# Performance work log

Hardware: AMD Instinct MI355X
Metric: run time of the kernel (lower is better)

The kernel has to match this reference:

```python
import jax, jax.numpy as jnp
import numpy as np

N, D, E = 200000, 256, 6400000
RATIO = 0.5
NEG_SLOPE = 0.2


def _xavier(key, shape, gain=1.414):
    fan_in, fan_out = shape[0], shape[1]
    limit = gain * (6.0 / (fan_in + fan_out)) ** 0.5
    return jax.random.uniform(key, shape, jnp.float32, -limit, limit)


def setup_inputs() -> dict:
    key = jax.random.key(0)
    ks = jax.random.split(key, 8)
    x = jax.random.normal(ks[0], (N, D), jnp.float32)
    edge_index = jax.random.randint(ks[1], (2, E), 0, N, dtype=jnp.int64)
    return {
        "x": x,
        "edge_index": edge_index,
        "w_s1": _xavier(ks[2], (2 * D, D)), "b_s1": jnp.zeros((D,), jnp.float32),
        "w_s2": _xavier(ks[3], (D, 1)),     "b_s2": jnp.zeros((1,), jnp.float32),
        "w_f1": _xavier(ks[4], (D, D // 2)), "b_f1": jnp.zeros((D // 2,), jnp.float32),
        "w_f2": _xavier(ks[5], (D // 2, 1)), "b_f2": jnp.zeros((1,), jnp.float32),
        "w_p": _xavier(ks[6], (D, D)),      "b_p": jnp.zeros((D,), jnp.float32),
        "alpha": jnp.float32(0.5), "beta": jnp.float32(0.5),
    }


def reference(x, edge_index, w_s1, b_s1, w_s2, b_s2, w_f1, b_f1, w_f2, b_f2, w_p, b_p, alpha, beta):
    num_nodes = x.shape[0]
    k = max(1, int(RATIO * num_nodes))
    lrelu = lambda v: jax.nn.leaky_relu(v, NEG_SLOPE)

    row, col = edge_index[0], edge_index[1]
    # degree(row, N): scatter-add of ones over source nodes
    deg = jax.ops.segment_sum(jnp.ones_like(row, dtype=x.dtype), row, num_segments=num_nodes)
    # F.normalize(p=2, dim=0) on the [N,1] degree column
    deg_norm = deg / jnp.maximum(jnp.sqrt(jnp.sum(deg * deg)), 1e-12)

    struct_in = jnp.concatenate([x, jnp.broadcast_to(deg_norm[:, None], x.shape)], axis=1)  # [N, 2D]
    struct_scores = (lrelu(struct_in @ w_s1 + b_s1) @ w_s2 + b_s2)[:, 0]  # dropout is eval no-op
    feat_scores = (lrelu(x @ w_f1 + b_f1) @ w_f2 + b_f2)[:, 0]

    a = jax.nn.sigmoid(alpha)
    b = jax.nn.sigmoid(beta)
    s = a + b
    scores = (a / s) * struct_scores + (b / s) * feat_scores  # [N]

    # single-graph top-k (batch=None default path)
    topk_scores, topk_idx = jax.lax.top_k(scores, k)
    x_pooled = lrelu(x[topk_idx] @ w_p + b_p)  # post_pool, dropout no-op

    # edge remap + compaction (valid edges first, -1 padding to keep static shape)
    node_map = jnp.full((num_nodes,), -1, dtype=jnp.int32).at[topk_idx].set(
        jnp.arange(k, dtype=jnp.int32))
    mr, mc = node_map[row], node_map[col]
    mask = (mr >= 0) & (mc >= 0)
    order = jnp.argsort(~mask, stable=True)  # stable: keeps original edge order among valid
    edge_index_pooled = jnp.stack([
        jnp.where(mask, mr, -1)[order],
        jnp.where(mask, mc, -1)[order],
    ])
    return x_pooled, edge_index_pooled, topk_scores
```

## Files before the change

### kernel.cpp

```cpp
#include <hip/hip_runtime.h>
#include <math.h>

typedef unsigned long long u64;
typedef unsigned int u32;
typedef unsigned short u16;
typedef __attribute__((ext_vector_type(8))) short bf16x8;
typedef __attribute__((ext_vector_type(4))) float f32x4;

#define D   256
#define ECH 16
#define EBLK (256*ECH)
#define BAND_W 4096
#define BAND_DELTA 1e-3f
#define HR  12544
#define HCH 32

__device__ __forceinline__ double lrelu(double v){ return v > 0.0 ? v : 0.2*v; }
__device__ __forceinline__ float  lreluf(float v){ return v > 0.0f ? v : 0.2f*v; }

__device__ __forceinline__ u16 f2bf(float f){
  union{float f; u32 u;} v; v.f = f;
  u32 r = v.u + 0x7FFFu + ((v.u >> 16) & 1u);
  return (u16)(r >> 16);
}
__device__ __forceinline__ float bf2f(u16 b){
  union{u32 u; float f;} v; v.u = ((u32)b) << 16; return v.f;
}

__global__ __launch_bounds__(256) void k_deghist(const int* __restrict__ row, int E,
                                                 u32* __restrict__ partial, int NR){
  __shared__ u32 h[HR];
  const int tid = threadIdx.x;
  const int r = blockIdx.x % NR;
  const int c = blockIdx.x / NR;
  for (int i = tid; i < HR; i += 256) h[i] = 0;
  __syncthreads();
  const int lo = r * HR;
  int CE = ((E + HCH - 1) / HCH + 3) & ~3;
  const int e0 = c * CE;
  const int e1 = min(e0 + CE, E);
  for (int e = e0 + tid*4; e < e1; e += 256*4){
    if (e + 3 < e1){
      int4 v = *(const int4*)(row + e);
      u32 d0 = (u32)(v.x - lo), d1 = (u32)(v.y - lo);
      u32 d2 = (u32)(v.z - lo), d3 = (u32)(v.w - lo);
      if (d0 < (u32)HR) atomicAdd(&h[d0], 1u);
      if (d1 < (u32)HR) atomicAdd(&h[d1], 1u);
      if (d2 < (u32)HR) atomicAdd(&h[d2], 1u);
      if (d3 < (u32)HR) atomicAdd(&h[d3], 1u);
    } else {
      for (int j = 0; j < 4 && e + j < e1; ++j){
        u32 d = (u32)(row[e+j] - lo);
        if (d < (u32)HR) atomicAdd(&h[d], 1u);
      }
    }
  }
  __syncthreads();
  u32* plane = partial + (size_t)blockIdx.x * HR;
  for (int i = tid; i < HR; i += 256) plane[i] = h[i];
}

__global__ void k_degred2(const u32* __restrict__ partial, int N, int NR,
                          int* __restrict__ deg, u64* __restrict__ out){
  __shared__ u64 sh[256];
  u64 local = 0;
  int stride = gridDim.x*blockDim.x;
  for (int i = blockIdx.x*blockDim.x + threadIdx.x; i < N; i += stride){
    int r = i / HR, off = i % HR;
    u32 s = 0;
    #pragma unroll 8
    for (int c = 0; c < HCH; ++c) s += partial[(size_t)(c*NR + r)*HR + off];
    deg[i] = (int)s;
    local += (u64)s * (u64)s;
  }
  sh[threadIdx.x] = local; __syncthreads();
  for (int s = 128; s > 0; s >>= 1){
    if (threadIdx.x < s) sh[threadIdx.x] += sh[threadIdx.x+s];
    __syncthreads();
  }
  if (threadIdx.x == 0) atomicAdd(out, sh[0]);
}

__global__ void k_prep(const float* __restrict__ wS1, const float* __restrict__ alpha,
                       const float* __restrict__ beta, const u64* __restrict__ sumsq,
                       double* __restrict__ s1b, double* __restrict__ scal,
                       float* __restrict__ s1bf, float* __restrict__ scalf){
  int j = threadIdx.x;
  double s = 0.0;
  for (int r = 0; r < D; ++r) s += (double)wS1[(D + r)*D + j];
  s1b[j] = s;
  s1bf[j] = (float)s;
  if (j == 0){
    double a = 1.0/(1.0 + exp(-(double)alpha[0]));
    double b = 1.0/(1.0 + exp(-(double)beta[0]));
    scal[0] = a/(a+b);
    scal[1] = b/(a+b);
    double dn = sqrt((double)(*sumsq));
    scal[2] = dn > 1e-12 ? dn : 1e-12;
    scalf[0] = (float)scal[0];
    scalf[1] = (float)scal[1];
    scalf[2] = (float)(1.0/scal[2]);
  }
}

__global__ void k_wsw(const float* __restrict__ wS1, const float* __restrict__ wF1,
                      u16* __restrict__ wswH, u16* __restrict__ wswL){
  int idx = blockIdx.x*blockDim.x + threadIdx.x;
  int i    = idx & 7;
  int lane = (idx >> 3) & 63;
  int sg   = (idx >> 9) & 7;
  int t    = idx >> 12;
  int k = sg*32 + ((lane >> 4) & 3)*8 + i;
  int c16 = lane & 15;
  float wv;
  if (t < 16) wv = wS1[k*256 + t*16 + c16];
  else        wv = wF1[k*128 + (t-16)*16 + c16];
  u16 h = f2bf(wv);
  float lo = wv - bf2f(h);
  wswH[idx] = h;
  wswL[idx] = f2bf(lo);
}

__global__ void k_wswP(const float* __restrict__ wP,
                       u16* __restrict__ wH, u16* __restrict__ wL){
  int idx = blockIdx.x*blockDim.x + threadIdx.x;
  int i    = idx & 7;
  int lane = (idx >> 3) & 63;
  int sg   = (idx >> 9) & 7;
  int t    = idx >> 12;
  int k = sg*32 + ((lane >> 4) & 3)*8 + i;
  float wv = wP[k*256 + t*16 + (lane & 15)];
  u16 h = f2bf(wv);
  float lo = wv - bf2f(h);
  wH[idx] = h;
  wL[idx] = f2bf(lo);
}

__global__ __launch_bounds__(512, 4) void k_scores_mfma(
    const float* __restrict__ x, const int* __restrict__ deg,
    const u16* __restrict__ wswH, const u16* __restrict__ wswL,
    const float* __restrict__ bS1, const float* __restrict__ wS2, const float* __restrict__ bS2,
    const float* __restrict__ bF1, const float* __restrict__ wF2, const float* __restrict__ bF2,
    const float* __restrict__ s1bf, const float* __restrict__ scalf,
    float* __restrict__ s32, u64* __restrict__ keys, int N)
{
  __shared__ u16 xsh[2][4096];
  __shared__ u16 xsl[2][4096];
  __shared__ float dnsh[64];
  __shared__ float part_s[64][9];
  __shared__ float part_f[64][9];

  const int tid  = threadIdx.x;
  const int lane = tid & 63;
  const int w    = tid >> 6;
  const int node0 = blockIdx.x * 64;

  if (tid < 64){
    int node = node0 + tid;
    dnsh[tid] = (node < N) ? ((float)deg[node] * scalf[2]) : 0.0f;
  }

  const int row_st = tid >> 3;
  const int seg_st = tid & 7;
  const int unit_w = row_st*8 + (seg_st ^ (row_st & 7));
  const float* srcbase = x + (size_t)(node0 + row_st)*D + seg_st*8;
  const bool rv = (node0 + row_st) < N;

  f32x4 acc[4][3];
  #pragma unroll
  for (int m = 0; m < 4; ++m)
    #pragma unroll
    for (int n = 0; n < 3; ++n) acc[m][n] = (f32x4){0.f,0.f,0.f,0.f};

  float xr[8];
  {
    if (rv){
      float4 a = *(const float4*)(srcbase);
      float4 b = *(const float4*)(srcbase + 4);
      xr[0]=a.x; xr[1]=a.y; xr[2]=a.z; xr[3]=a.w;
      xr[4]=b.x; xr[5]=b.y; xr[6]=b.z; xr[7]=b.w;
    } else {
      #pragma unroll
      for (int i = 0; i < 8; ++i) xr[i] = 0.f;
    }
  }

  #pragma unroll
  for (int c = 0; c < 4; ++c){
    const int pb = c & 1;
    {
      u16 h[8];
      #pragma unroll
      for (int i = 0; i < 8; ++i) h[i] = f2bf(xr[i]);
      uint4 H; H.x = (u32)h[0] | ((u32)h[1]<<16); H.y = (u32)h[2] | ((u32)h[3]<<16);
               H.z = (u32)h[4] | ((u32)h[5]<<16); H.w = (u32)h[6] | ((u32)h[7]<<16);
      u16 l[8];
      #pragma unroll
      for (int i = 0; i < 8; ++i) l[i] = f2bf(xr[i] - bf2f(h[i]));
      uint4 L; L.x = (u32)l[0] | ((u32)l[1]<<16); L.y = (u32)l[2] | ((u32)l[3]<<16);
               L.z = (u32)l[4] | ((u32)l[5]<<16); L.w = (u32)l[6] | ((u32)l[7]<<16);
      *(uint4*)&xsh[pb][unit_w*8] = H;
      *(uint4*)&xsl[pb][unit_w*8] = L;
    }
    if (c < 3){
      const float* sn = srcbase + (c+1)*64;
      if (rv){
        float4 a = *(const float4*)(sn);
        float4 b = *(const float4*)(sn + 4);
        xr[0]=a.x; xr[1]=a.y; xr[2]=a.z; xr[3]=a.w;
        xr[4]=b.x; xr[5]=b.y; xr[6]=b.z; xr[7]=b.w;
      }
    }
    __syncthreads();
    #pragma unroll
    for (int s = 0; s < 2; ++s){
      const int sg = c*2 + s;
      bf16x8 ah[4], al[4];
      #pragma unroll
      for (int mt = 0; mt < 4; ++mt){
        int row = mt*16 + (lane & 15);
        int seg = s*4 + (lane >> 4);
        int un  = row*8 + (seg ^ (row & 7));
        ah[mt] = *(const bf16x8*)&xsh[pb][un*8];
        al[mt] = *(const bf16x8*)&xsl[pb][un*8];
      }
      const int t0 = w*3;
      size_t o0 = ((size_t)(t0*8 + sg)*64 + lane)*8;
      bf16x8 bh = *(const bf16x8*)&wswH[o0];
      bf16x8 bl = *(const bf16x8*)&wswL[o0];
      #pragma unroll
      for (int nt = 0; nt < 3; ++nt){
        bf16x8 nbh = bh, nbl = bl;
        if (nt < 2){
          size_t on = ((size_t)((t0+nt+1)*8 + sg)*64 + lane)*8;
          nbh = *(const bf16x8*)&wswH[on];
          nbl = *(const bf16x8*)&wswL[on];
        }
        #pragma unroll
        for (int mt = 0; mt < 4; ++mt){
          acc[mt][nt] = __builtin_amdgcn_mfma_f32_16x16x32_bf16(ah[mt], bh, acc[mt][nt], 0,0,0);
          acc[mt][nt] = __builtin_amdgcn_mfma_f32_16x16x32_bf16(al[mt], bh, acc[mt][nt], 0,0,0);
          acc[mt][nt] = __builtin_amdgcn_mfma_f32_16x16x32_bf16(ah[mt], bl, acc[mt][nt], 0,0,0);
        }
        bh = nbh; bl = nbl;
      }
    }
    __syncthreads();
  }

  float dnl[4][4];
  #pragma unroll
  for (int mt = 0; mt < 4; ++mt)
    #pragma unroll
    for (int j = 0; j < 4; ++j)
      dnl[mt][j] = dnsh[mt*16 + (lane>>4)*4 + j];

  float ps[4][4], pf[4][4];
  #pragma unroll
  for (int mt = 0; mt < 4; ++mt)
    #pragma unroll
    for (int j = 0; j < 4; ++j){ ps[mt][j] = 0.f; pf[mt][j] = 0.f; }

  #pragma unroll
  for (int nt = 0; nt < 3; ++nt){
    const int t = w*3 + nt;
    const int c16 = lane & 15;
    const bool isS = (t < 16);
    const int col = isS ? t*16 + c16 : (t-16)*16 + c16;
    const float bias = isS ? bS1[col] : bF1[col];
    const float sbv  = isS ? s1bf[col] : 0.f;
    const float vv   = isS ? wS2[col] : wF2[col];
    #pragma unroll
    for (int mt = 0; mt < 4; ++mt){
      #pragma unroll
      for (int j = 0; j < 4; ++j){
        float v = acc[mt][nt][j] + bias + dnl[mt][j]*sbv;
        v = lreluf(v) * vv;
        v += __shfl_xor(v, 1);
        v += __shfl_xor(v, 2);
        v += __shfl_xor(v, 4);
        v += __shfl_xor(v, 8);
        if (isS) ps[mt][j] += v; else pf[mt][j] += v;
      }
    }
  }
  if ((lane & 15) == 0){
    #pragma unroll
    for (int mt = 0; mt < 4; ++mt)
      #pragma unroll
      for (int j = 0; j < 4; ++j){
        int row = mt*16 + (lane>>4)*4 + j;
        part_s[row][w] = ps[mt][j];
        part_f[row][w] = pf[mt][j];
      }
  }
  __syncthreads();
  if (tid < 64){
    int node = node0 + tid;
    if (node < N){
      float sv = 0.f, fv = 0.f;
      #pragma unroll
      for (int ww = 0; ww < 8; ++ww){ sv += part_s[tid][ww]; fv += part_f[tid][ww]; }
      float sc = scalf[0]*(sv + bS2[0]) + scalf[1]*(fv + bF2[0]);
      s32[node] = sc;
      u32 bits = __float_as_uint(sc);
      u32 ord = (bits >> 31) ? ~bits : (bits | 0x80000000u);
      keys[node] = ((u64)(~ord) << 32) | (u32)node;
    }
  }
}

__global__ void k_padkeys(u64* __restrict__ keys, int N, int SORTN){
  int i = N + blockIdx.x*blockDim.x + threadIdx.x;
  if (i < SORTN) keys[i] = ~0ULL;
}

__global__ __launch_bounds__(1024) void k_bsort_local8k(u64* __restrict__ keys){
  __shared__ u64 sk[8192];
  const int tid = threadIdx.x;
  const int base = blockIdx.x * 8192;
  #pragma unroll
  for (int e = 0; e < 8; ++e) sk[tid + e*1024] = keys[base + tid + e*1024];
  __syncthreads();
  for (int size = 2; size <= 8192; size <<= 1){
    for (int stride = size >> 1; stride > 0; stride >>= 1){
      #pragma unroll
      for (int pp = 0; pp < 4; ++pp){
        int p  = tid + pp*1024;
        int i  = 2*p - (p & (stride-1));
        int jj = i + stride;
        bool up = (((base + i) & size) == 0);
        u64 ki = sk[i], kj = sk[jj];
        if ((ki > kj) == up){ sk[i] = kj; sk[jj] = ki; }
      }
      __syncthreads();
    }
  }
  #pragma unroll
  for (int e = 0; e < 8; ++e) keys[base + tid + e*1024] = sk[tid + e*1024];
}

__global__ __launch_bounds__(1024) void k_bmerge_local8k(u64* __restrict__ keys, int size){
  __shared__ u64 sk[8192];
  const int tid = threadIdx.x;
  const int base = blockIdx.x * 8192;
  #pragma unroll
  for (int e = 0; e < 8; ++e) sk[tid + e*1024] = keys[base + tid + e*1024];
  __syncthreads();
  for (int stride = 4096; stride > 0; stride >>= 1){
    #pragma unroll
    for (int pp = 0; pp < 4; ++pp){
      int p  = tid + pp*1024;
      int i  = 2*p - (p & (stride-1));
      int jj = i + stride;
      bool up = (((base + i) & size) == 0);
      u64 ki = sk[i], kj = sk[jj];
      if ((ki > kj) == up){ sk[i] = kj; sk[jj] = ki; }
    }
    __syncthreads();
  }
  #pragma unroll
  for (int e = 0; e < 8; ++e) keys[base + tid + e*1024] = sk[tid + e*1024];
}

template<int NS>
__global__ void k_bpassM(u64* __restrict__ keys, int size, int stride){
  const int G = 1 << NS;
  u32 t = blockIdx.x*blockDim.x + threadIdx.x;
  u32 smin = (u32)stride >> (NS-1);
  u32 i0 = (t/smin)*(smin << NS) + (t % smin);
  u64 v[G];
  #pragma unroll
  for (int j = 0; j < G; ++j) v[j] = keys[i0 + (u32)j*smin];
  bool up = ((i0 & (u32)size) == 0);
  #pragma unroll
  for (int b = (G>>1); b >= 1; b >>= 1){
    #pragma unroll
    for (int j = 0; j < G; ++j){
      if ((j & b) == 0){
        u64 a = v[j], cc = v[j|b];
        if ((a > cc) == up){ v[j] = cc; v[j|b] = a; }
      }
    }
  }
  #pragma unroll
  for (int j = 0; j < G; ++j) keys[i0 + (u32)j*smin] = v[j];
}

__global__ void kr_cut(const u64* __restrict__ keys, int k, float* __restrict__ cutbuf,
                       int* __restrict__ r01){
  if (threadIdx.x == 0 && blockIdx.x == 0){
    u32 key32 = (u32)(keys[k-1] >> 32);
    u32 ord = ~key32;
    u32 u = (ord & 0x80000000u) ? (ord ^ 0x80000000u) : ~ord;
    float c = __uint_as_float(u);
    cutbuf[0] = c - BAND_DELTA;
    cutbuf[1] = c + BAND_DELTA;
    r01[0] = 0x7FFFFFFF;
    r01[1] = -1;
  }
}

__global__ __launch_bounds__(256) void kr_rescore(
    const u64* __restrict__ keys, const float* __restrict__ s32,
    const float* __restrict__ x, const int* __restrict__ deg,
    const float* __restrict__ wS1, const float* __restrict__ bS1,
    const float* __restrict__ wS2, const float* __restrict__ bS2,
    const float* __restrict__ wF1, const float* __restrict__ bF1,
    const float* __restrict__ wF2, const float* __restrict__ bF2,
    const double* __restrict__ s1b, const double* __restrict__ scal,
    const float* __restrict__ cutbuf, int* __restrict__ r01,
    double* __restrict__ bandS, int k, int N)
{
  const int r = k - BAND_W + blockIdx.x;
  if (r < 0 || r >= N) return;
  const int node = (int)(u32)(keys[r] & 0xFFFFFFFFULL);
  const float s = s32[node];
  if (s < cutbuf[0] || s > cutbuf[1]) return;

  const int tid = threadIdx.x;
  if (tid == 0){ atomicMin(&r01[0], r); atomicMax(&r01[1], r); }

  __shared__ float xr[256];
  __shared__ double rsp[4], rfp[4];
  xr[tid] = x[(size_t)node*D + tid];
  __syncthreads();

  const int j = tid;
  double accA = (double)bS1[j] + ((double)deg[node]/scal[2]) * s1b[j];
  double accB = (j < 128) ? (double)bF1[j] : 0.0;
  for (int rr = 0; rr < D; ++rr){
    double xv = (double)xr[rr];
    accA = fma(xv, (double)wS1[rr*D + j], accA);
    if (j < 128) accB = fma(xv, (double)wF1[rr*128 + j], accB);
  }
  double sp = lrelu(accA) * (double)wS2[j];
  double fp = (j < 128) ? lrelu(accB) * (double)wF2[j] : 0.0;

  const int lane = tid & 63, wave = tid >> 6;
  #pragma unroll
  for (int off = 32; off > 0; off >>= 1){
    sp += __shfl_down(sp, off);
    fp += __shfl_down(fp, off);
  }
  if (lane == 0){ rsp[wave] = sp; rfp[wave] = fp; }
  __syncthreads();
  if (tid == 0){
    double SP = rsp[0]+rsp[1]+rsp[2]+rsp[3];
    double FP = rfp[0]+rfp[1]+rfp[2]+rfp[3];
    bandS[blockIdx.x] = scal[0]*(SP + (double)bS2[0]) + scal[1]*(FP + (double)bF2[0]);
  }
}

__global__ __launch_bounds__(1024) void kr_bandsort(u64* __restrict__ keys,
    const double* __restrict__ bandS, const int* __restrict__ r01, int k){
  __shared__ double bs[8192];
  __shared__ int bi[8192];
  const int r0 = r01[0], r1 = r01[1];
  int nb = r1 - r0 + 1;
  if (nb <= 1) return;
  if (nb > 8192) nb = 8192;
  int M = 1; while (M < nb) M <<= 1;
  const int tid = threadIdx.x;
  const int sbase = r0 - (k - BAND_W);
  for (int m = tid; m < M; m += 1024){
    if (m < nb){ bs[m] = bandS[sbase + m]; bi[m] = (int)(u32)(keys[r0+m] & 0xFFFFFFFFULL); }
    else       { bs[m] = -1.0/0.0;         bi[m] = 0x7FFFFFFF; }
  }
  __syncthreads();
  for (int size = 2; size <= M; size <<= 1){
    for (int stride = size >> 1; stride > 0; stride >>= 1){
      for (int p = tid; p < (M >> 1); p += 1024){
        int i = 2*p - (p & (stride-1));
        int jj = i + stride;
        bool up = ((i & size) == 0);
        double si_ = bs[i], sj = bs[jj];
        int ii = bi[i], ij = bi[jj];
        bool gt = (si_ < sj) || (si_ == sj && ii > ij);
        if (gt == up){ bs[i]=sj; bs[jj]=si_; bi[i]=ij; bi[jj]=ii; }
      }
      __syncthreads();
    }
  }
  for (int m = tid; m < nb; m += 1024)
    keys[r0+m] = (u64)(u32)bi[m];
}

__global__ void k_finalize(const u64* __restrict__ keys, const float* __restrict__ s32,
                           int k, int* __restrict__ nmap, float* __restrict__ outS){
  int p = blockIdx.x*blockDim.x + threadIdx.x;
  if (p < k){
    int node = (int)(u32)(keys[p] & 0xFFFFFFFFULL);
    nmap[node] = p;
    outS[p] = s32[node];
  }
}

__global__ __launch_bounds__(512, 4) void k_xpool_mfma(
    const float* __restrict__ x, const u64* __restrict__ keys,
    const u16* __restrict__ wH, const u16* __restrict__ wL,
    const float* __restrict__ bP, float* __restrict__ out, int kk)
{
  __shared__ u16 xsh[2][4096];
  __shared__ u16 xsl[2][4096];

  const int tid  = threadIdx.x;
  const int lane = tid & 63;
  const int w    = tid >> 6;
  const int p0 = blockIdx.x * 64;
  if (p0 >= kk) return;

  const int row_st = tid >> 3;
  const int seg_st = tid & 7;
  const int unit_w = row_st*8 + (seg_st ^ (row_st & 7));
  int prow = p0 + row_st; if (prow >= kk) prow = kk - 1;
  const int node = (int)(u32)(keys[prow] & 0xFFFFFFFFULL);
  const float* srcbase = x + (size_t)node*D + seg_st*8;

  f32x4 acc[4][2];
  #pragma unroll
  for (int m = 0; m < 4; ++m){ acc[m][0] = (f32x4){0.f,0.f,0.f,0.f}; acc[m][1] = (f32x4){0.f,0.f,0.f,0.f}; }

  float xr[8];
  {
    float4 a = *(const float4*)(srcbase);
    float4 b = *(const float4*)(srcbase + 4);
    xr[0]=a.x; xr[1]=a.y; xr[2]=a.z; xr[3]=a.w;
    xr[4]=b.x; xr[5]=b.y; xr[6]=b.z; xr[7]=b.w;
  }

  #pragma unroll
  for (int c = 0; c < 4; ++c){
    const int pb = c & 1;
    {
      u16 h[8];
      #pragma unroll
      for (int i = 0; i < 8; ++i) h[i] = f2bf(xr[i]);
      uint4 H; H.x = (u32)h[0] | ((u32)h[1]<<16); H.y = (u32)h[2] | ((u32)h[3]<<16);
               H.z = (u32)h[4] | ((u32)h[5]<<16); H.w = (u32)h[6] | ((u32)h[7]<<16);
      u16 l[8];
      #pragma unroll
      for (int i = 0; i < 8; ++i) l[i] = f2bf(xr[i] - bf2f(h[i]));
      uint4 L; L.x = (u32)l[0] | ((u32)l[1]<<16); L.y = (u32)l[2] | ((u32)l[3]<<16);
               L.z = (u32)l[4] | ((u32)l[5]<<16); L.w = (u32)l[6] | ((u32)l[7]<<16);
      *(uint4*)&xsh[pb][unit_w*8] = H;
      *(uint4*)&xsl[pb][unit_w*8] = L;
    }
    if (c < 3){
      const float* sn = srcbase + (c+1)*64;
      float4 a = *(const float4*)(sn);
      float4 b = *(const float4*)(sn + 4);
      xr[0]=a.x; xr[1]=a.y; xr[2]=a.z; xr[3]=a.w;
      xr[4]=b.x; xr[5]=b.y; xr[6]=b.z; xr[7]=b.w;
    }
    __syncthreads();
    #pragma unroll
    for (int s = 0; s < 2; ++s){
      const int sg = c*2 + s;
      bf16x8 ah[4], al[4];
      #pragma unroll
      for (int mt = 0; mt < 4; ++mt){
        int row = mt*16 + (lane & 15);
        int seg = s*4 + (lane >> 4);
        int un  = row*8 + (seg ^ (row & 7));
        ah[mt] = *(const bf16x8*)&xsh[pb][un*8];
        al[mt] = *(const bf16x8*)&xsl[pb][un*8];
      }
      const int t0 = w*2;
      size_t o0 = ((size_t)(t0*8 + sg)*64 + lane)*8;
      bf16x8 bh = *(const bf16x8*)&wH[o0];
      bf16x8 bl = *(const bf16x8*)&wL[o0];
      #pragma unroll
      for (int nt = 0; nt < 2; ++nt){
        bf16x8 nbh = bh, nbl = bl;
        if (nt < 1){
          size_t on = ((size_t)((t0+1)*8 + sg)*64 + lane)*8;
          nbh = *(const bf16x8*)&wH[on];
          nbl = *(const bf16x8*)&wL[on];
        }
        #pragma unroll
        for (int mt = 0; mt < 4; ++mt){
          acc[mt][nt] = __builtin_amdgcn_mfma_f32_16x16x32_bf16(ah[mt], bh, acc[mt][nt], 0,0,0);
          acc[mt][nt] = __builtin_amdgcn_mfma_f32_16x16x32_bf16(al[mt], bh, acc[mt][nt], 0,0,0);
          acc[mt][nt] = __builtin_amdgcn_mfma_f32_16x16x32_bf16(ah[mt], bl, acc[mt][nt], 0,0,0);
        }
        bh = nbh; bl = nbl;
      }
    }
    __syncthreads();
  }

  const int c16 = lane & 15, r4 = (lane >> 4)*4;
  #pragma unroll
  for (int nt = 0; nt < 2; ++nt){
    const int col = (w*2 + nt)*16 + c16;
    const float bias = bP[col];
    #pragma unroll
    for (int mt = 0; mt < 4; ++mt){
      #pragma unroll
      for (int j = 0; j < 4; ++j){
        int p = p0 + mt*16 + r4 + j;
        if (p < kk) out[(size_t)p*D + col] = lreluf(acc[mt][nt][j] + bias);
      }
    }
  }
}

__global__ __launch_bounds__(256) void k_ecount(const int* __restrict__ erow, const int* __restrict__ ecol,
    const int* __restrict__ nmap, int E, int* __restrict__ bcount){
  __shared__ int sc[256];
  const int tid = threadIdx.x;
  const int base = blockIdx.x*EBLK + tid*ECH;
  int cnt = 0;
  #pragma unroll
  for (int q = 0; q < ECH; ++q){
    int e = base + q;
    if (e < E){
      if (nmap[erow[e]] >= 0 && nmap[ecol[e]] >= 0) cnt++;
    }
  }
  sc[tid] = cnt; __syncthreads();
  for (int s = 128; s > 0; s >>= 1){
    if (tid < s) sc[tid] += sc[tid+s];
    __syncthreads();
  }
  if (tid == 0) bcount[blockIdx.x] = sc[0];
}

__global__ __launch_bounds__(1024) void k_escan(const int* __restrict__ bcount, int nblk,
                                                int* __restrict__ boff, int* __restrict__ tot){
  __shared__ int sh[1024];
  const int tid = threadIdx.x;
  int carry = 0;
  for (int s = 0; s < nblk; s += 1024){
    int v = (s + tid < nblk) ? bcount[s+tid] : 0;
    sh[tid] = v; __syncthreads();
    for (int d = 1; d < 1024; d <<= 1){
      int t = (tid >= d) ? sh[tid-d] : 0;
      __syncthreads();
      sh[tid] += t;
      __syncthreads();
    }
    if (s + tid < nblk) boff[s+tid] = carry + sh[tid] - v;
    carry += sh[1023];
    __syncthreads();
  }
  if (tid == 0) *tot = carry;
}

__global__ void k_efill_tail(float* __restrict__ outR, float* __restrict__ outC,
                             const int* __restrict__ tot, int E){
  const int t0 = *tot;
  int stride = gridDim.x*blockDim.x;
  for (int i = t0 + blockIdx.x*blockDim.x + threadIdx.x; i < E; i += stride){
    outR[i] = -1.0f;
    outC[i] = -1.0f;
  }
}

__global__ __launch_bounds__(256) void k_escatter(const int* __restrict__ erow, const int* __restrict__ ecol,
    const int* __restrict__ nmap, int E, const int* __restrict__ boff,
    float* __restrict__ outR, float* __restrict__ outC){
  __shared__ int sc[256];
  const int tid = threadIdx.x;
  const int base = blockIdx.x*EBLK + tid*ECH;
  int mr[ECH], mc[ECH];
  int cnt = 0;
  #pragma unroll
  for (int q = 0; q < ECH; ++q){
    int e = base + q;
    int a = -1, b = -1;
    if (e < E){ a = nmap[erow[e]]; b = nmap[ecol[e]]; }
    mr[q] = a; mc[q] = b;
    if (a >= 0 && b >= 0) cnt++;
  }
  sc[tid] = cnt; __syncthreads();
  int v = cnt;
  for (int d = 1; d < 256; d <<= 1){
    int t = (tid >= d) ? sc[tid-d] : 0;
    __syncthreads();
    sc[tid] += t;
    __syncthreads();
  }
  int pos = boff[blockIdx.x] + sc[tid] - v;
  #pragma unroll
  for (int q = 0; q < ECH; ++q){
    if (mr[q] >= 0 && mc[q] >= 0){
      outR[pos] = (float)mr[q];
      outC[pos] = (float)mc[q];
      pos++;
    }
  }
}

extern "C" void kernel_launch(void* const* d_in, const int* in_sizes, int n_in,
                              void* d_out, int out_size, void* d_ws, size_t ws_size,
                              hipStream_t stream)
{
  const float* x   = (const float*)d_in[0];
  const int*   ei  = (const int*)d_in[1];
  const float* wS1 = (const float*)d_in[2];
  const float* bS1 = (const float*)d_in[3];
  const float* wS2 = (const float*)d_in[4];
  const float* bS2 = (const float*)d_in[5];
  const float* wF1 = (const float*)d_in[6];
  const float* bF1 = (const float*)d_in[7];
  const float* wF2 = (const float*)d_in[8];
  const float* bF2 = (const float*)d_in[9];
  const float* wP  = (const float*)d_in[10];
  const float* bP  = (const float*)d_in[11];
  const float* alpha = (const float*)d_in[12];
  const float* beta  = (const float*)d_in[13];
  (void)n_in; (void)out_size; (void)ws_size;

  const int N = in_sizes[0] / D;
  const int E = in_sizes[1] / 2;
  int k = (int)(0.5 * (double)N); if (k < 1) k = 1;
  int SORTN = 8192; while (SORTN < N) SORTN <<= 1;
  const int nblk_e = (E + EBLK - 1) / EBLK;
  const int NR = (N + HR - 1) / HR;

  char* w = (char*)d_ws;
  size_t off = 0;
  auto alloc = [&](size_t bytes)->char*{
    char* p = w + off;
    off = (off + bytes + 255) & ~(size_t)255;
    return p;
  };
  float*  s32    = (float*) alloc((size_t)N*4);
  u64*    keys   = (u64*)   alloc((size_t)SORTN*8);
  int*    deg    = (int*)   alloc((size_t)N*4);
  int*    nmap   = (int*)   alloc((size_t)N*4);
  double* s1b    = (double*)alloc((size_t)D*8);
  float*  s1bf   = (float*) alloc((size_t)D*4);
  double* scal   = (double*)alloc(4*8);
  float*  scalf  = (float*) alloc(4*4);
  u64*    sumsq  = (u64*)   alloc(8);
  float*  cutbuf = (float*) alloc(2*4);
  int*    r01    = (int*)   alloc(2*4);
  int*    tot    = (int*)   alloc(4);
  double* bandS  = (double*)alloc((size_t)2*BAND_W*8);
  u16*    wswH   = (u16*)   alloc((size_t)98304*2);
  u16*    wswL   = (u16*)   alloc((size_t)98304*2);
  u16*    wswPH  = (u16*)   alloc((size_t)65536*2);
  u16*    wswPL  = (u16*)   alloc((size_t)65536*2);
  int*    bcount = (int*)   alloc((size_t)nblk_e*4);
  int*    boff   = (int*)   alloc((size_t)nblk_e*4);

  float* outX  = (float*)d_out;
  float* outER = outX  + (size_t)k*D;
  float* outEC = outER + (size_t)E;
  float* outS  = outEC + (size_t)E;

  u32* partial = (u32*)outER;

  hipMemsetAsync(sumsq, 0,    8,           stream);
  hipMemsetAsync(nmap,  0xFF, (size_t)N*4, stream);

  k_deghist<<<NR*HCH, 256, 0, stream>>>(ei, E, partial, NR);
  k_degred2<<<1024, 256, 0, stream>>>(partial, N, NR, deg, sumsq);
  k_prep   <<<1,    D,   0, stream>>>(wS1, alpha, beta, sumsq, s1b, scal, s1bf, scalf);
  k_wsw    <<<384,  256, 0, stream>>>(wS1, wF1, wswH, wswL);
  k_wswP   <<<256,  256, 0, stream>>>(wP, wswPH, wswPL);
  k_scores_mfma<<<(N + 63)/64, 512, 0, stream>>>(x, deg, wswH, wswL,
                                                 bS1, wS2, bS2, bF1, wF2, bF2,
                                                 s1bf, scalf, s32, keys, N);
  k_padkeys<<<(SORTN - N + 255)/256, 256, 0, stream>>>(keys, N, SORTN);

  k_bsort_local8k<<<SORTN/8192, 1024, 0, stream>>>(keys);
  for (int size = 16384; size <= SORTN; size <<= 1){
    int stride = size >> 1;
    while (stride >= 8192){
      int ns = 1;
      while (ns < 4 && (stride >> ns) >= 8192) ns++;
      switch (ns){
        case 1: k_bpassM<1><<<SORTN/2/256,  256, 0, stream>>>(keys, size, stride); break;
        case 2: k_bpassM<2><<<SORTN/4/256,  256, 0, stream>>>(keys, size, stride); break;
        case 3: k_bpassM<3><<<SORTN/8/256,  256, 0, stream>>>(keys, size, stride); break;
        default:k_bpassM<4><<<SORTN/16/256, 256, 0, stream>>>(keys, size, stride); break;
      }
      stride >>= ns;
    }
    k_bmerge_local8k<<<SORTN/8192, 1024, 0, stream>>>(keys, size);
  }

  kr_cut     <<<1, 64, 0, stream>>>(keys, k, cutbuf, r01);
  kr_rescore <<<2*BAND_W, 256, 0, stream>>>(keys, s32, x, deg, wS1,bS1,wS2,bS2,
                                            wF1,bF1,wF2,bF2, s1b, scal,
                                            cutbuf, r01, bandS, k, N);
  kr_bandsort<<<1, 1024, 0, stream>>>(keys, bandS, r01, k);

  k_finalize<<<(k+255)/256, 256, 0, stream>>>(keys, s32, k, nmap, outS);
  k_xpool_mfma<<<(k+63)/64, 512, 0, stream>>>(x, keys, wswPH, wswPL, bP, outX, k);
  k_ecount  <<<nblk_e, 256, 0, stream>>>(ei, ei+E, nmap, E, bcount);
  k_escan   <<<1, 1024, 0, stream>>>(bcount, nblk_e, boff, tot);
  k_efill_tail<<<1024, 256, 0, stream>>>(outER, outEC, tot, E);
  k_escatter<<<nblk_e, 256, 0, stream>>>(ei, ei+E, nmap, E, boff, outER, outEC);
}
```

Measured before the change: 828.8 us.

## Stage full x tile in LDS once and use 2x4 warp grid for MFMA GEMMs

Both the score kernel and the post-pool projection kernel now load and split the whole 64x256 input tile into LDS in one pass with a single barrier, replacing the double-buffered four-chunk pipeline. Warps are rearranged from eight warps covering all 64 rows each to a 2x4 grid, each warp handling 32 rows and more output tiles. This halves per-warp global loads of the split weights and removes per-chunk barriers. In exchange, LDS use doubles to 64 KB per block, which may reduce occupancy, and load/compute overlap is lost.

Measured after the change: 850.5 us. +2.6%, slower.

```diff
diff --git a/kernel.cpp b/kernel.cpp
--- a/kernel.cpp
+++ b/kernel.cpp
@@ -144,15 +144,17 @@
     const float* __restrict__ s1bf, const float* __restrict__ scalf,
     float* __restrict__ s32, u64* __restrict__ keys, int N)
 {
-  __shared__ u16 xsh[2][4096];
-  __shared__ u16 xsl[2][4096];
+  __shared__ u16 xsh[4][4096];
+  __shared__ u16 xsl[4][4096];
   __shared__ float dnsh[64];
-  __shared__ float part_s[64][9];
-  __shared__ float part_f[64][9];
+  __shared__ float part_s[64][4];
+  __shared__ float part_f[64][4];
 
   const int tid  = threadIdx.x;
   const int lane = tid & 63;
   const int w    = tid >> 6;
+  const int g    = w >> 2;
+  const int q    = w & 3;
   const int node0 = blockIdx.x * 64;
 
   if (tid < 64){
@@ -160,147 +162,122 @@
     dnsh[tid] = (node < N) ? ((float)deg[node] * scalf[2]) : 0.0f;
   }
 
-  const int row_st = tid >> 3;
-  const int seg_st = tid & 7;
-  const int unit_w = row_st*8 + (seg_st ^ (row_st & 7));
-  const float* srcbase = x + (size_t)(node0 + row_st)*D + seg_st*8;
-  const bool rv = (node0 + row_st) < N;
-
-  f32x4 acc[4][3];
-  #pragma unroll
-  for (int m = 0; m < 4; ++m)
-    #pragma unroll
-    for (int n = 0; n < 3; ++n) acc[m][n] = (f32x4){0.f,0.f,0.f,0.f};
-
-  float xr[8];
   {
-    if (rv){
-      float4 a = *(const float4*)(srcbase);
-      float4 b = *(const float4*)(srcbase + 4);
-      xr[0]=a.x; xr[1]=a.y; xr[2]=a.z; xr[3]=a.w;
-      xr[4]=b.x; xr[5]=b.y; xr[6]=b.z; xr[7]=b.w;
-    } else {
+    const int row_st = tid >> 3;
+    const int seg_st = tid & 7;
+    const int unit   = row_st*8 + (seg_st ^ (row_st & 7));
+    const float* srcbase = x + (size_t)(node0 + row_st)*D + seg_st*8;
+    const bool rv = (node0 + row_st) < N;
+    #pragma unroll
+    for (int c = 0; c < 4; ++c){
+      float xr[8];
+      if (rv){
+        float4 a = *(const float4*)(srcbase + c*64);
+        float4 b = *(const float4*)(srcbase + c*64 + 4);
+        xr[0]=a.x; xr[1]=a.y; xr[2]=a.z; xr[3]=a.w;
+        xr[4]=b.x; xr[5]=b.y; xr[6]=b.z; xr[7]=b.w;
+      } else {
+        #pragma unroll
+        for (int i = 0; i < 8; ++i) xr[i] = 0.f;
+      }
+      u16 h[8], l[8];
       #pragma unroll
-      for (int i = 0; i < 8; ++i) xr[i] = 0.f;
-    }
-  }
-
-  #pragma unroll
-  for (int c = 0; c < 4; ++c){
-    const int pb = c & 1;
-    {
-      u16 h[8];
-      #pragma unroll
-      for (int i = 0; i < 8; ++i) h[i] = f2bf(xr[i]);
+      for (int i = 0; i < 8; ++i){ h[i] = f2bf(xr[i]); l[i] = f2bf(xr[i] - bf2f(h[i])); }
       uint4 H; H.x = (u32)h[0] | ((u32)h[1]<<16); H.y = (u32)h[2] | ((u32)h[3]<<16);
                H.z = (u32)h[4] | ((u32)h[5]<<16); H.w = (u32)h[6] | ((u32)h[7]<<16);
-      u16 l[8];
-      #pragma unroll
-      for (int i = 0; i < 8; ++i) l[i] = f2bf(xr[i] - bf2f(h[i]));
       uint4 L; L.x = (u32)l[0] | ((u32)l[1]<<16); L.y = (u32)l[2] | ((u32)l[3]<<16);
                L.z = (u32)l[4] | ((u32)l[5]<<16); L.w = (u32)l[6] | ((u32)l[7]<<16);
-      *(uint4*)&xsh[pb][unit_w*8] = H;
-      *(uint4*)&xsl[pb][unit_w*8] = L;
-    }
-    if (c < 3){
-      const float* sn = srcbase + (c+1)*64;
-      if (rv){
-        float4 a = *(const float4*)(sn);
-        float4 b = *(const float4*)(sn + 4);
-        xr[0]=a.x; xr[1]=a.y; xr[2]=a.z; xr[3]=a.w;
-        xr[4]=b.x; xr[5]=b.y; xr[6]=b.z; xr[7]=b.w;
-      }
-    }
-    __syncthreads();
-    #pragma unroll
-    for (int s = 0; s < 2; ++s){
-      const int sg = c*2 + s;
-      bf16x8 ah[4], al[4];
+      *(uint4*)&xsh[c][unit*8] = H;
+      *(uint4*)&xsl[c][unit*8] = L;
+    }
+  }
+  __syncthreads();
+
+  f32x4 acc[2][6];
+  #pragma unroll
+  for (int m = 0; m < 2; ++m)
+    #pragma unroll
+    for (int n = 0; n < 6; ++n) acc[m][n] = (f32x4){0.f,0.f,0.f,0.f};
+
+  #pragma unroll
+  for (int sg = 0; sg < 8; ++sg){
+    const int s = sg & 1, c = sg >> 1;
+    bf16x8 ah[2], al[2];
+    #pragma unroll
+    for (int m = 0; m < 2; ++m){
+      int row = (g*2 + m)*16 + (lane & 15);
+      int seg = s*4 + (lane >> 4);
+      int un  = row*8 + (seg ^ (row & 7));
+      ah[m] = *(const bf16x8*)&xsh[c][un*8];
+      al[m] = *(const bf16x8*)&xsl[c][un*8];
+    }
+    #pragma unroll
+    for (int nt = 0; nt < 6; ++nt){
+      const int t = q*6 + nt;
+      size_t o = ((size_t)(t*8 + sg)*64 + lane)*8;
+      bf16x8 bh = *(const bf16x8*)&wswH[o];
+      bf16x8 bl = *(const bf16x8*)&wswL[o];
       #pragma unroll
-      for (int mt = 0; mt < 4; ++mt){
-        int row = mt*16 + (lane & 15);
-        int seg = s*4 + (lane >> 4);
-        int un  = row*8 + (seg ^ (row & 7));
-        ah[mt] = *(const bf16x8*)&xsh[pb][un*8];
-        al[mt] = *(const bf16x8*)&xsl[pb][un*8];
-      }
-      const int t0 = w*3;
-      size_t o0 = ((size_t)(t0*8 + sg)*64 + lane)*8;
-      bf16x8 bh = *(const bf16x8*)&wswH[o0];
-      bf16x8 bl = *(const bf16x8*)&wswL[o0];
-      #pragma unroll
-      for (int nt = 0; nt < 3; ++nt){
-        bf16x8 nbh = bh, nbl = bl;
-        if (nt < 2){
-          size_t on = ((size_t)((t0+nt+1)*8 + sg)*64 + lane)*8;
-          nbh = *(const bf16x8*)&wswH[on];
-          nbl = *(const bf16x8*)&wswL[on];
-        }
-        #pragma unroll
-        for (int mt = 0; mt < 4; ++mt){
-          acc[mt][nt] = __builtin_amdgcn_mfma_f32_16x16x32_bf16(ah[mt], bh, acc[mt][nt], 0,0,0);
-          acc[mt][nt] = __builtin_amdgcn_mfma_f32_16x16x32_bf16(al[mt], bh, acc[mt][nt], 0,0,0);
-          acc[mt][nt] = __builtin_amdgcn_mfma_f32_16x16x32_bf16(ah[mt], bl, acc[mt][nt], 0,0,0);
-        }
-        bh = nbh; bl = nbl;
-      }
-    }
-    __syncthreads();
-  }
-
-  float dnl[4][4];
-  #pragma unroll
-  for (int mt = 0; mt < 4; ++mt)
+      for (int m = 0; m < 2; ++m){
+        acc[m][nt] = __builtin_amdgcn_mfma_f32_16x16x32_bf16(ah[m], bh, acc[m][nt], 0,0,0);
+        acc[m][nt] = __builtin_amdgcn_mfma_f32_16x16x32_bf16(al[m], bh, acc[m][nt], 0,0,0);
+        acc[m][nt] = __builtin_amdgcn_mfma_f32_16x16x32_bf16(ah[m], bl, acc[m][nt], 0,0,0);
+      }
+    }
+  }
+
+  const int c16 = lane & 15;
+  float dnl[2][4];
+  #pragma unroll
+  for (int m = 0; m < 2; ++m)
     #pragma unroll
     for (int j = 0; j < 4; ++j)
-      dnl[mt][j] = dnsh[mt*16 + (lane>>4)*4 + j];
-
-  float ps[4][4], pf[4][4];
-  #pragma unroll
-  for (int mt = 0; mt < 4; ++mt)
-    #pragma unroll
-    for (int j = 0; j < 4; ++j){ ps[mt][j] = 0.f; pf[mt][j] = 0.f; }
-
-  #pragma unroll
-  for (int nt = 0; nt < 3; ++nt){
-    const int t = w*3 + nt;
-    const int c16 = lane & 15;
+      dnl[m][j] = dnsh[(g*2 + m)*16 + (lane>>4)*4 + j];
+
+  float ps[2][4], pf[2][4];
+  #pragma unroll
+  for (int m = 0; m < 2; ++m)
+    #pragma unroll
+    for (int j = 0; j < 4; ++j){ ps[m][j] = 0.f; pf[m][j] = 0.f; }
+
+  #pragma unroll
+  for (int nt = 0; nt < 6; ++nt){
+    const int t = q*6 + nt;
     const bool isS = (t < 16);
     const int col = isS ? t*16 + c16 : (t-16)*16 + c16;
     const float bias = isS ? bS1[col] : bF1[col];
     const float sbv  = isS ? s1bf[col] : 0.f;
     const float vv   = isS ? wS2[col] : wF2[col];
     #pragma unroll
-    for (int mt = 0; mt < 4; ++mt){
+    for (int m = 0; m < 2; ++m){
       #pragma unroll
       for (int j = 0; j < 4; ++j){
-        float v = acc[mt][nt][j] + bias + dnl[mt][j]*sbv;
+        float v = acc[m][nt][j] + bias + dnl[m][j]*sbv;
         v = lreluf(v) * vv;
         v += __shfl_xor(v, 1);
         v += __shfl_xor(v, 2);
         v += __shfl_xor(v, 4);
         v += __shfl_xor(v, 8);
-        if (isS) ps[mt][j] += v; else pf[mt][j] += v;
-      }
-    }
-  }
-  if ((lane & 15) == 0){
-    #pragma unroll
-    for (int mt = 0; mt < 4; ++mt)
+        if (isS) ps[m][j] += v; else pf[m][j] += v;
+      }
+    }
+  }
+  if (c16 == 0){
+    #pragma unroll
+    for (int m = 0; m < 2; ++m)
       #pragma unroll
       for (int j = 0; j < 4; ++j){
-        int row = mt*16 + (lane>>4)*4 + j;
-        part_s[row][w] = ps[mt][j];
-        part_f[row][w] = pf[mt][j];
+        int row = (g*2 + m)*16 + (lane>>4)*4 + j;
+        part_s[row][q] = ps[m][j];
+        part_f[row][q] = pf[m][j];
       }
   }
   __syncthreads();
   if (tid < 64){
     int node = node0 + tid;
     if (node < N){
-      float sv = 0.f, fv = 0.f;
-      #pragma unroll
-      for (int ww = 0; ww < 8; ++ww){ sv += part_s[tid][ww]; fv += part_f[tid][ww]; }
+      float sv = part_s[tid][0] + part_s[tid][1] + part_s[tid][2] + part_s[tid][3];
+      float fv = part_f[tid][0] + part_f[tid][1] + part_f[tid][2] + part_f[tid][3];
       float sc = scalf[0]*(sv + bS2[0]) + scalf[1]*(fv + bF2[0]);
       s32[node] = sc;
       u32 bits = __float_as_uint(sc);
@@ -501,106 +478,86 @@
     const u16* __restrict__ wH, const u16* __restrict__ wL,
     const float* __restrict__ bP, float* __restrict__ out, int kk)
 {
-  __shared__ u16 xsh[2][4096];
-  __shared__ u16 xsl[2][4096];
+  __shared__ u16 xsh[4][4096];
+  __shared__ u16 xsl[4][4096];
 
   const int tid  = threadIdx.x;
   const int lane = tid & 63;
   const int w    = tid >> 6;
+  const int g    = w >> 2;
+  const int q    = w & 3;
   const int p0 = blockIdx.x * 64;
   if (p0 >= kk) return;
 
-  const int row_st = tid >> 3;
-  const int seg_st = tid & 7;
-  const int unit_w = row_st*8 + (seg_st ^ (row_st & 7));
-  int prow = p0 + row_st; if (prow >= kk) prow = kk - 1;
-  const int node = (int)(u32)(keys[prow] & 0xFFFFFFFFULL);
-  const float* srcbase = x + (size_t)node*D + seg_st*8;
-
-  f32x4 acc[4][2];
-  #pragma unroll
-  for (int m = 0; m < 4; ++m){ acc[m][0] = (f32x4){0.f,0.f,0.f,0.f}; acc[m][1] = (f32x4){0.f,0.f,0.f,0.f}; }
-
-  float xr[8];
   {
-    float4 a = *(const float4*)(srcbase);
-    float4 b = *(const float4*)(srcbase + 4);
-    xr[0]=a.x; xr[1]=a.y; xr[2]=a.z; xr[3]=a.w;
-    xr[4]=b.x; xr[5]=b.y; xr[6]=b.z; xr[7]=b.w;
-  }
-
-  #pragma unroll
-  for (int c = 0; c < 4; ++c){
-    const int pb = c & 1;
-    {
-      u16 h[8];
+    const int row_st = tid >> 3;
+    const int seg_st = tid & 7;
+    const int unit   = row_st*8 + (seg_st ^ (row_st & 7));
+    int prow = p0 + row_st; if (prow >= kk) prow = kk - 1;
+    const int node = (int)(u32)(keys[prow] & 0xFFFFFFFFULL);
+    const float* srcbase = x + (size_t)node*D + seg_st*8;
+    #pragma unroll
+    for (int c = 0; c < 4; ++c){
+      float4 a = *(const float4*)(srcbase + c*64);
+      float4 b = *(const float4*)(srcbase + c*64 + 4);
+      float xr[8] = {a.x,a.y,a.z,a.w, b.x,b.y,b.z,b.w};
+      u16 h[8], l[8];
       #pragma unroll
-      for (int i = 0; i < 8; ++i) h[i] = f2bf(xr[i]);
+      for (int i = 0; i < 8; ++i){ h[i] = f2bf(xr[i]); l[i] = f2bf(xr[i] - bf2f(h[i])); }
       uint4 H; H.x = (u32)h[0] | ((u32)h[1]<<16); H.y = (u32)h[2] | ((u32)h[3]<<16);
                H.z = (u32)h[4] | ((u32)h[5]<<16); H.w = (u32)h[6] | ((u32)h[7]<<16);
-      u16 l[8];
-      #pragma unroll
-      for (int i = 0; i < 8; ++i) l[i] = f2bf(xr[i] - bf2f(h[i]));
       uint4 L; L.x = (u32)l[0] | ((u32)l[1]<<16); L.y = (u32)l[2] | ((u32)l[3]<<16);
                L.z = (u32)l[4] | ((u32)l[5]<<16); L.w = (u32)l[6] | ((u32)l[7]<<16);
-      *(uint4*)&xsh[pb][unit_w*8] = H;
-      *(uint4*)&xsl[pb][unit_w*8] = L;
-    }
-    if (c < 3){
-      const float* sn = srcbase + (c+1)*64;
-      float4 a = *(const float4*)(sn);
-      float4 b = *(const float4*)(sn + 4);
-      xr[0]=a.x; xr[1]=a.y; xr[2]=a.z; xr[3]=a.w;
-      xr[4]=b.x; xr[5]=b.y; xr[6]=b.z; xr[7]=b.w;
-    }
-    __syncthreads();
-    #pragma unroll
-    for (int s = 0; s < 2; ++s){
-      const int sg = c*2 + s;
-      bf16x8 ah[4], al[4];
+      *(uint4*)&xsh[c][unit*8] = H;
+      *(uint4*)&xsl[c][unit*8] = L;
+    }
+  }
+  __syncthreads();
+
+  f32x4 acc[2][4];
+  #pragma unroll
+  for (int m = 0; m < 2; ++m)
+    #pragma unroll
+    for (int n = 0; n < 4; ++n) acc[m][n] = (f32x4){0.f,0.f,0.f,0.f};
+
+  #pragma unroll
+  for (int sg = 0; sg < 8; ++sg){
+    const int s = sg & 1, c = sg >> 1;
+    bf16x8 ah[2], al[2];
+    #pragma unroll
+    for (int m = 0; m < 2; ++m){
+      int row = (g*2 + m)*16 + (lane & 15);
+      int seg = s*4 + (lane >> 4);
+      int un  = row*8 + (seg ^ (row & 7));
+      ah[m] = *(const bf16x8*)&xsh[c][un*8];
+      al[m] = *(const bf16x8*)&xsl[c][un*8];
+    }
+    #pragma unroll
+    for (int nt = 0; nt < 4; ++nt){
+      const int t = q*4 + nt;
+      size_t o = ((size_t)(t*8 + sg)*64 + lane)*8;
+      bf16x8 bh = *(const bf16x8*)&wH[o];
+      bf16x8 bl = *(const bf16x8*)&wL[o];
       #pragma unroll
-      for (int mt = 0; mt < 4; ++mt){
-        int row = mt*16 + (lane & 15);
-        int seg = s*4 + (lane >> 4);
-        int un  = row*8 + (seg ^ (row & 7));
-        ah[mt] = *(const bf16x8*)&xsh[pb][un*8];
-        al[mt] = *(const bf16x8*)&xsl[pb][un*8];
-      }
-      const int t0 = w*2;
-      size_t o0 = ((size_t)(t0*8 + sg)*64 + lane)*8;
-      bf16x8 bh = *(const bf16x8*)&wH[o0];
-      bf16x8 bl = *(const bf16x8*)&wL[o0];
-      #pragma unroll
-      for (int nt = 0; nt < 2; ++nt){
-        bf16x8 nbh = bh, nbl = bl;
-        if (nt < 1){
-          size_t on = ((size_t)((t0+1)*8 + sg)*64 + lane)*8;
-          nbh = *(const bf16x8*)&wH[on];
-          nbl = *(const bf16x8*)&wL[on];
-        }
-        #pragma unroll
-        for (int mt = 0; mt < 4; ++mt){
-          acc[mt][nt] = __builtin_amdgcn_mfma_f32_16x16x32_bf16(ah[mt], bh, acc[mt][nt], 0,0,0);
-          acc[mt][nt] = __builtin_amdgcn_mfma_f32_16x16x32_bf16(al[mt], bh, acc[mt][nt], 0,0,0);
-          acc[mt][nt] = __builtin_amdgcn_mfma_f32_16x16x32_bf16(ah[mt], bl, acc[mt][nt], 0,0,0);
-        }
-        bh = nbh; bl = nbl;
-      }
-    }
-    __syncthreads();
+      for (int m = 0; m < 2; ++m){
+        acc[m][nt] = __builtin_amdgcn_mfma_f32_16x16x32_bf16(ah[m], bh, acc[m][nt], 0,0,0);
+        acc[m][nt] = __builtin_amdgcn_mfma_f32_16x16x32_bf16(al[m], bh, acc[m][nt], 0,0,0);
+        acc[m][nt] = __builtin_amdgcn_mfma_f32_16x16x32_bf16(ah[m], bl, acc[m][nt], 0,0,0);
+      }
+    }
   }
 
   const int c16 = lane & 15, r4 = (lane >> 4)*4;
   #pragma unroll
-  for (int nt = 0; nt < 2; ++nt){
-    const int col = (w*2 + nt)*16 + c16;
+  for (int nt = 0; nt < 4; ++nt){
+    const int col = (q*4 + nt)*16 + c16;
     const float bias = bP[col];
     #pragma unroll
-    for (int mt = 0; mt < 4; ++mt){
+    for (int m = 0; m < 2; ++m){
       #pragma unroll
       for (int j = 0; j < 4; ++j){
-        int p = p0 + mt*16 + r4 + j;
-        if (p < kk) out[(size_t)p*D + col] = lreluf(acc[mt][nt][j] + bias);
+        int p = p0 + (g*2 + m)*16 + r4 + j;
+        if (p < kk) out[(size_t)p*D + col] = lreluf(acc[m][nt][j] + bias);
       }
     }
   }
```
